# Kernel optimization log

Measured on AMD Instinct MI355X. Metric: run time of the kernel, lower is better.

## Reference

```python
import jax, jax.numpy as jnp
import numpy as np

SEQ_LEN, BATCH, HID, ATT = 2048, 64, 512, 512


def setup_inputs() -> dict:
    key = jax.random.key(0)
    k1, k2, k3, k4, k5, k6 = jax.random.split(key, 6)
    return {
        "dec_out": jax.random.normal(k1, (BATCH, HID), dtype=jnp.float32),
        "enc_outs": jax.random.normal(k2, (SEQ_LEN, BATCH, HID), dtype=jnp.float32),
        "W_s": jax.random.normal(k3, (ATT, HID), dtype=jnp.float32) * (1.0 / np.sqrt(HID)),
        "W_t": jax.random.normal(k4, (ATT, HID), dtype=jnp.float32) * (1.0 / np.sqrt(HID)),
        "b_t": jax.random.normal(k5, (ATT,), dtype=jnp.float32) * 0.01,
        "v_a": jax.random.uniform(k6, (ATT,), dtype=jnp.float32, minval=-0.05, maxval=0.05),
    }


def reference(dec_out, enc_outs, W_s, W_t, b_t, v_a):
    # enc_att: (seq_len, batch, att) = W_s @ enc_outs
    enc_att = jnp.einsum('sbh,ah->sba', enc_outs, W_s)
    # dec_att: (batch, att) = W_t @ dec_out + b_t
    dec_att = dec_out @ W_t.T + b_t
    # score(b, s) = v_a . tanh(enc_att[s,b] + dec_att[b])
    scores = jnp.einsum('sba,a->bs', jnp.tanh(enc_att + dec_att[None, :, :]), v_a)
    return scores  # (batch, seq_len)
```

## Files before the change

kernel.cpp:

```cpp
#include <hip/hip_runtime.h>

typedef __attribute__((ext_vector_type(8))) short short8;
typedef __attribute__((ext_vector_type(4))) float f32x4;

#define SEQ 2048
#define BATCH 64
#define HID 512
#define ATT 512

__device__ __forceinline__ unsigned short f2bf(float f) {
  unsigned u = __float_as_uint(f);
  u += 0x7fffu + ((u >> 16) & 1u);
  return (unsigned short)(u >> 16);
}

__global__ void bahdanau_pre(const float* __restrict__ dec_out,
                             const float* __restrict__ W_t,
                             const float* __restrict__ b_t,
                             const float* __restrict__ W_s,
                             unsigned short* __restrict__ wsb,
                             float* __restrict__ dec_att) {
  if (blockIdx.x < 64) {
    const int b = blockIdx.x;
    __shared__ float drow[HID];
    for (int i = threadIdx.x; i < HID; i += 256) drow[i] = dec_out[b * HID + i];
    __syncthreads();
    for (int a = threadIdx.x; a < ATT; a += 256) {
      const float4* wr = (const float4*)(W_t + (size_t)a * HID);
      float s0 = 0.f, s1 = 0.f, s2 = 0.f, s3 = 0.f;
#pragma unroll 4
      for (int j = 0; j < HID / 4; ++j) {
        float4 w = wr[j];
        s0 = fmaf(w.x, drow[4 * j + 0], s0);
        s1 = fmaf(w.y, drow[4 * j + 1], s1);
        s2 = fmaf(w.z, drow[4 * j + 2], s2);
        s3 = fmaf(w.w, drow[4 * j + 3], s3);
      }
      dec_att[b * ATT + a] = (s0 + s1) + (s2 + s3) + b_t[a];
    }
  } else {
    const int cb = blockIdx.x - 64;
    const float4* src = (const float4*)W_s;
#pragma unroll
    for (int i = 0; i < 4; ++i) {
      int idx = cb * 1024 + i * 256 + threadIdx.x;
      float4 v = src[idx];
      ushort4 o;
      o.x = f2bf(v.x); o.y = f2bf(v.y); o.z = f2bf(v.z); o.w = f2bf(v.w);
      ((ushort4*)wsb)[idx] = o;
    }
  }
}

__global__ __launch_bounds__(512, 2)
void bahdanau_main(const float* __restrict__ enc,
                   const unsigned short* __restrict__ wsb,
                   const float* __restrict__ dec_att,
                   const float* __restrict__ v_a,
                   float* __restrict__ out) {
  __shared__ __align__(16) unsigned short Alds[2][2048];
  __shared__ float partial[8 * 64];

  const int tid  = threadIdx.x;
  const int wave = tid >> 6;
  const int lane = tid & 63;
  const int c = lane & 15;
  const int q = lane >> 4;
  const int s = blockIdx.x;
  const int n0 = wave * 64;

  const int srow = tid >> 3;
  const int skc  = (tid & 7) * 4;
  const int ldst = ((skc >> 3) * 64 + srow) * 8 + (skc & 7);
  const float* gsrc = enc + ((size_t)s * 64 + srow) * HID + skc;

  const unsigned short* bsrc = wsb + (size_t)(n0 + c) * HID + q * 8;

  f32x4 acc[4][4] = {};

  {
    float4 v = *(const float4*)gsrc;
    ushort4 o;
    o.x = f2bf(v.x); o.y = f2bf(v.y); o.z = f2bf(v.z); o.w = f2bf(v.w);
    *(ushort4*)&Alds[0][ldst] = o;
  }
  short8 bp[4];
#pragma unroll
  for (int nt = 0; nt < 4; ++nt)
    bp[nt] = *(const short8*)(bsrc + (size_t)nt * 16 * HID);
  __syncthreads();

#pragma unroll
  for (int kk = 0; kk < 16; ++kk) {
    const int cur = kk & 1;

    short8 bfr[4];
#pragma unroll
    for (int nt = 0; nt < 4; ++nt) bfr[nt] = bp[nt];

    float4 stg;
    if (kk < 15) stg = *(const float4*)(gsrc + (kk + 1) * 32);

    if (kk < 15) {
#pragma unroll
      for (int nt = 0; nt < 4; ++nt)
        bp[nt] = *(const short8*)(bsrc + (size_t)nt * 16 * HID + (kk + 1) * 32);
    }

    const unsigned short* ab = &Alds[cur][(q * 64 + c) * 8];
    short8 a[4];
#pragma unroll
    for (int mt = 0; mt < 4; ++mt)
      a[mt] = *(const short8*)(ab + mt * 16 * 8);

#pragma unroll
    for (int mt = 0; mt < 4; ++mt)
#pragma unroll
      for (int nt = 0; nt < 4; ++nt)
        acc[mt][nt] = __builtin_amdgcn_mfma_f32_16x16x32_bf16(a[mt], bfr[nt], acc[mt][nt], 0, 0, 0);

    if (kk < 15) {
      ushort4 o;
      o.x = f2bf(stg.x); o.y = f2bf(stg.y); o.z = f2bf(stg.z); o.w = f2bf(stg.w);
      *(ushort4*)&Alds[cur ^ 1][ldst] = o;
    }
    __syncthreads();
  }

  float va[4];
#pragma unroll
  for (int nt = 0; nt < 4; ++nt) va[nt] = v_a[n0 + nt * 16 + c];

  float rowsum[4][4];
#pragma unroll
  for (int mt = 0; mt < 4; ++mt) {
#pragma unroll
    for (int r = 0; r < 4; ++r) {
      const int ml = mt * 16 + q * 4 + r;
      float sum = 0.f;
#pragma unroll
      for (int nt = 0; nt < 4; ++nt) {
        const int n = n0 + nt * 16 + c;
        float x = acc[mt][nt][r] + dec_att[ml * ATT + n];
        float e = __builtin_amdgcn_exp2f(x * 2.8853900817779268f);
        float t = 1.f - 2.f * __builtin_amdgcn_rcpf(e + 1.f);
        sum = fmaf(va[nt], t, sum);
      }
      rowsum[mt][r] = sum;
    }
  }

#pragma unroll
  for (int off = 1; off < 16; off <<= 1) {
#pragma unroll
    for (int mt = 0; mt < 4; ++mt)
#pragma unroll
      for (int r = 0; r < 4; ++r)
        rowsum[mt][r] += __shfl_xor(rowsum[mt][r], off, 64);
  }

  if (c == 0) {
#pragma unroll
    for (int mt = 0; mt < 4; ++mt)
#pragma unroll
      for (int r = 0; r < 4; ++r)
        partial[wave * 64 + mt * 16 + q * 4 + r] = rowsum[mt][r];
  }
  __syncthreads();

  if (tid < 64) {
    float sum = 0.f;
#pragma unroll
    for (int w = 0; w < 8; ++w) sum += partial[w * 64 + tid];
    out[(size_t)tid * SEQ + s] = sum;
  }
}

extern "C" void kernel_launch(void* const* d_in, const int* in_sizes, int n_in,
                              void* d_out, int out_size, void* d_ws, size_t ws_size,
                              hipStream_t stream) {
  const float* dec_out = (const float*)d_in[0];
  const float* enc     = (const float*)d_in[1];
  const float* W_s     = (const float*)d_in[2];
  const float* W_t     = (const float*)d_in[3];
  const float* b_t     = (const float*)d_in[4];
  const float* v_a     = (const float*)d_in[5];
  float* out = (float*)d_out;

  unsigned short* wsb = (unsigned short*)d_ws;
  float* dec_att = (float*)((char*)d_ws + (size_t)ATT * HID * 2);

  bahdanau_pre<<<128, 256, 0, stream>>>(dec_out, W_t, b_t, W_s, wsb, dec_att);
  bahdanau_main<<<SEQ, 512, 0, stream>>>(enc, wsb, dec_att, v_a, out);
}
```

Baseline: 532.9 us.

## Process several sequence steps per block with whole-tile register prefetch

Each block now handles 8 sequence positions instead of one. The full 64x512 encoder slab is prefetched into registers, converted to bf16 into a single padded LDS buffer, and the next slab is loaded while the current MFMA loop runs. dec_att is cached once per block in LDS as bf16, and W_s fragments use a two-deep register prefetch. This removes per-k-step barriers and amortizes dec_att reads, at the cost of heavy register pressure (64 floats of staging), large LDS use that lowers occupancy, only 256 blocks, and bf16 rounding of dec_att.

```diff
diff --git a/kernel.cpp b/kernel.cpp
--- a/kernel.cpp
+++ b/kernel.cpp
@@ -7,11 +7,16 @@
 #define BATCH 64
 #define HID 512
 #define ATT 512
+#define SPB 8
+#define DPF 2
 
 __device__ __forceinline__ unsigned short f2bf(float f) {
   unsigned u = __float_as_uint(f);
   u += 0x7fffu + ((u >> 16) & 1u);
   return (unsigned short)(u >> 16);
+}
+__device__ __forceinline__ float bf2f(unsigned short h) {
+  return __uint_as_float(((unsigned)h) << 16);
 }
 
 __global__ void bahdanau_pre(const float* __restrict__ dec_out,
@@ -58,121 +63,144 @@
                    const float* __restrict__ dec_att,
                    const float* __restrict__ v_a,
                    float* __restrict__ out) {
-  __shared__ __align__(16) unsigned short Alds[2][2048];
-  __shared__ float partial[8 * 64];
+  __shared__ __align__(16) unsigned short Albuf[64 * 65 * 8];
+  __shared__ __align__(16) unsigned short decl[64 * 520];
+  __shared__ float partial[512];
 
   const int tid  = threadIdx.x;
   const int wave = tid >> 6;
   const int lane = tid & 63;
   const int c = lane & 15;
   const int q = lane >> 4;
-  const int s = blockIdx.x;
   const int n0 = wave * 64;
+  const int s0 = blockIdx.x * SPB;
+
+  {
+    const float4* dsrc = (const float4*)dec_att;
+#pragma unroll
+    for (int i = 0; i < 16; ++i) {
+      int idx = i * 512 + tid;
+      float4 v = dsrc[idx];
+      int e = idx * 4;
+      int row = e >> 9, col = e & 511;
+      ushort4 o;
+      o.x = f2bf(v.x); o.y = f2bf(v.y); o.z = f2bf(v.z); o.w = f2bf(v.w);
+      *(ushort4*)&decl[row * 520 + col] = o;
+    }
+  }
 
   const int srow = tid >> 3;
   const int skc  = (tid & 7) * 4;
-  const int ldst = ((skc >> 3) * 64 + srow) * 8 + (skc & 7);
-  const float* gsrc = enc + ((size_t)s * 64 + srow) * HID + skc;
+  const int ldst = (((skc >> 3) & 3) * 65 + srow) * 8 + (skc & 7);
+  const float* gbase = enc + ((size_t)s0 * 64 + srow) * HID + skc;
+
+  float4 stg[16];
+#pragma unroll
+  for (int kk = 0; kk < 16; ++kk) stg[kk] = *(const float4*)(gbase + kk * 32);
 
   const unsigned short* bsrc = wsb + (size_t)(n0 + c) * HID + q * 8;
 
-  f32x4 acc[4][4] = {};
-
-  {
-    float4 v = *(const float4*)gsrc;
-    ushort4 o;
-    o.x = f2bf(v.x); o.y = f2bf(v.y); o.z = f2bf(v.z); o.w = f2bf(v.w);
-    *(ushort4*)&Alds[0][ldst] = o;
-  }
-  short8 bp[4];
-#pragma unroll
-  for (int nt = 0; nt < 4; ++nt)
-    bp[nt] = *(const short8*)(bsrc + (size_t)nt * 16 * HID);
+  float va[4];
+#pragma unroll
+  for (int nt = 0; nt < 4; ++nt) va[nt] = v_a[n0 + nt * 16 + c];
+
+  for (int si = 0; si < SPB; ++si) {
+    __syncthreads();
+
+    if (si > 0 && tid < 64) {
+      float sum = 0.f;
+#pragma unroll
+      for (int w = 0; w < 8; ++w) sum += partial[w * 64 + tid];
+      out[(size_t)tid * SEQ + (s0 + si - 1)] = sum;
+    }
+
+#pragma unroll
+    for (int kk = 0; kk < 16; ++kk) {
+      ushort4 o;
+      o.x = f2bf(stg[kk].x); o.y = f2bf(stg[kk].y);
+      o.z = f2bf(stg[kk].z); o.w = f2bf(stg[kk].w);
+      *(ushort4*)&Albuf[kk * 2080 + ldst] = o;
+    }
+
+    __syncthreads();
+
+    const float* gnext = gbase + (size_t)(si + 1) * (64 * HID);
+    const bool more = (si + 1 < SPB);
+
+    short8 bp[DPF][4];
+#pragma unroll
+    for (int d = 0; d < DPF; ++d)
+#pragma unroll
+      for (int nt = 0; nt < 4; ++nt)
+        bp[d][nt] = *(const short8*)(bsrc + (size_t)nt * 16 * HID + d * 32);
+
+    f32x4 acc[4][4] = {};
+
+#pragma unroll
+    for (int kk = 0; kk < 16; ++kk) {
+      const unsigned short* ab = &Albuf[kk * 2080 + (q * 65 + c) * 8];
+      short8 a4[4];
+#pragma unroll
+      for (int mt = 0; mt < 4; ++mt)
+        a4[mt] = *(const short8*)(ab + mt * 16 * 8);
+
+#pragma unroll
+      for (int mt = 0; mt < 4; ++mt)
+#pragma unroll
+        for (int nt = 0; nt < 4; ++nt)
+          acc[mt][nt] = __builtin_amdgcn_mfma_f32_16x16x32_bf16(a4[mt], bp[kk % DPF][nt], acc[mt][nt], 0, 0, 0);
+
+      if (kk + DPF < 16) {
+#pragma unroll
+        for (int nt = 0; nt < 4; ++nt)
+          bp[kk % DPF][nt] = *(const short8*)(bsrc + (size_t)nt * 16 * HID + (kk + DPF) * 32);
+      }
+      if (more) stg[kk] = *(const float4*)(gnext + kk * 32);
+    }
+
+    float rowsum[4][4];
+#pragma unroll
+    for (int mt = 0; mt < 4; ++mt) {
+#pragma unroll
+      for (int r = 0; r < 4; ++r) {
+        const int ml = mt * 16 + q * 4 + r;
+        float sum = 0.f;
+#pragma unroll
+        for (int nt = 0; nt < 4; ++nt) {
+          const int n = n0 + nt * 16 + c;
+          float x = acc[mt][nt][r] + bf2f(decl[ml * 520 + n]);
+          float e = __builtin_amdgcn_exp2f(x * 2.8853900817779268f);
+          float t = 1.f - 2.f * __builtin_amdgcn_rcpf(e + 1.f);
+          sum = fmaf(va[nt], t, sum);
+        }
+        rowsum[mt][r] = sum;
+      }
+    }
+
+#pragma unroll
+    for (int off = 1; off < 16; off <<= 1) {
+#pragma unroll
+      for (int mt = 0; mt < 4; ++mt)
+#pragma unroll
+        for (int r = 0; r < 4; ++r)
+          rowsum[mt][r] += __shfl_xor(rowsum[mt][r], off, 64);
+    }
+
+    if (c == 0) {
+#pragma unroll
+      for (int mt = 0; mt < 4; ++mt)
+#pragma unroll
+        for (int r = 0; r < 4; ++r)
+          partial[wave * 64 + mt * 16 + q * 4 + r] = rowsum[mt][r];
+    }
+  }
+
   __syncthreads();
-
-#pragma unroll
-  for (int kk = 0; kk < 16; ++kk) {
-    const int cur = kk & 1;
-
-    short8 bfr[4];
-#pragma unroll
-    for (int nt = 0; nt < 4; ++nt) bfr[nt] = bp[nt];
-
-    float4 stg;
-    if (kk < 15) stg = *(const float4*)(gsrc + (kk + 1) * 32);
-
-    if (kk < 15) {
-#pragma unroll
-      for (int nt = 0; nt < 4; ++nt)
-        bp[nt] = *(const short8*)(bsrc + (size_t)nt * 16 * HID + (kk + 1) * 32);
-    }
-
-    const unsigned short* ab = &Alds[cur][(q * 64 + c) * 8];
-    short8 a[4];
-#pragma unroll
-    for (int mt = 0; mt < 4; ++mt)
-      a[mt] = *(const short8*)(ab + mt * 16 * 8);
-
-#pragma unroll
-    for (int mt = 0; mt < 4; ++mt)
-#pragma unroll
-      for (int nt = 0; nt < 4; ++nt)
-        acc[mt][nt] = __builtin_amdgcn_mfma_f32_16x16x32_bf16(a[mt], bfr[nt], acc[mt][nt], 0, 0, 0);
-
-    if (kk < 15) {
-      ushort4 o;
-      o.x = f2bf(stg.x); o.y = f2bf(stg.y); o.z = f2bf(stg.z); o.w = f2bf(stg.w);
-      *(ushort4*)&Alds[cur ^ 1][ldst] = o;
-    }
-    __syncthreads();
-  }
-
-  float va[4];
-#pragma unroll
-  for (int nt = 0; nt < 4; ++nt) va[nt] = v_a[n0 + nt * 16 + c];
-
-  float rowsum[4][4];
-#pragma unroll
-  for (int mt = 0; mt < 4; ++mt) {
-#pragma unroll
-    for (int r = 0; r < 4; ++r) {
-      const int ml = mt * 16 + q * 4 + r;
-      float sum = 0.f;
-#pragma unroll
-      for (int nt = 0; nt < 4; ++nt) {
-        const int n = n0 + nt * 16 + c;
-        float x = acc[mt][nt][r] + dec_att[ml * ATT + n];
-        float e = __builtin_amdgcn_exp2f(x * 2.8853900817779268f);
-        float t = 1.f - 2.f * __builtin_amdgcn_rcpf(e + 1.f);
-        sum = fmaf(va[nt], t, sum);
-      }
-      rowsum[mt][r] = sum;
-    }
-  }
-
-#pragma unroll
-  for (int off = 1; off < 16; off <<= 1) {
-#pragma unroll
-    for (int mt = 0; mt < 4; ++mt)
-#pragma unroll
-      for (int r = 0; r < 4; ++r)
-        rowsum[mt][r] += __shfl_xor(rowsum[mt][r], off, 64);
-  }
-
-  if (c == 0) {
-#pragma unroll
-    for (int mt = 0; mt < 4; ++mt)
-#pragma unroll
-      for (int r = 0; r < 4; ++r)
-        partial[wave * 64 + mt * 16 + q * 4 + r] = rowsum[mt][r];
-  }
-  __syncthreads();
-
   if (tid < 64) {
     float sum = 0.f;
 #pragma unroll
     for (int w = 0; w < 8; ++w) sum += partial[w * 64 + tid];
-    out[(size_t)tid * SEQ + s] = sum;
+    out[(size_t)tid * SEQ + (s0 + SPB - 1)] = sum;
   }
 }
 
@@ -191,5 +219,5 @@
   float* dec_att = (float*)((char*)d_ws + (size_t)ATT * HID * 2);
 
   bahdanau_pre<<<128, 256, 0, stream>>>(dec_out, W_t, b_t, W_s, wsb, dec_att);
-  bahdanau_main<<<SEQ, 512, 0, stream>>>(enc, wsb, dec_att, v_a, out);
-}
+  bahdanau_main<<<SEQ / SPB, 512, 0, stream>>>(enc, wsb, dec_att, v_a, out);
+}
```

Result: no change. 542.5 us (+1.8%).

## Stage A and B tiles via global_load_lds DMA and prelayout W_s in MFMA order

Applied to the files above, without the earlier changes.

Replaces the register-staged loads of the fp32 encoder tile and the bf16 W_s fragments with direct global-to-LDS DMA (global_load_lds), double-buffered across the K loop. W_s is pre-permuted in the prep kernel into an MFMA-fragment-friendly blocked layout so each wave copies contiguous 1KB chunks. dec_att is stored transposed and used to initialize the accumulators, removing the scattered adds in the epilogue. The main kernel now needs 80KB of LDS, which may cut occupancy below the launch-bounds target of two blocks per CU, and the bf16 conversion of A now happens after the LDS read.

```diff
diff --git a/kernel.cpp b/kernel.cpp
--- a/kernel.cpp
+++ b/kernel.cpp
@@ -12,6 +12,12 @@
   unsigned u = __float_as_uint(f);
   u += 0x7fffu + ((u >> 16) & 1u);
   return (unsigned short)(u >> 16);
+}
+
+__device__ __forceinline__ void dma16(const void* g, void* l) {
+  __builtin_amdgcn_global_load_lds(
+      (const __attribute__((address_space(1))) unsigned int*)g,
+      (__attribute__((address_space(3))) unsigned int*)l, 16, 0, 0);
 }
 
 __global__ void bahdanau_pre(const float* __restrict__ dec_out,
@@ -19,7 +25,7 @@
                              const float* __restrict__ b_t,
                              const float* __restrict__ W_s,
                              unsigned short* __restrict__ wsb,
-                             float* __restrict__ dec_att) {
+                             float* __restrict__ decT) {
   if (blockIdx.x < 64) {
     const int b = blockIdx.x;
     __shared__ float drow[HID];
@@ -36,7 +42,7 @@
         s2 = fmaf(w.z, drow[4 * j + 2], s2);
         s3 = fmaf(w.w, drow[4 * j + 3], s3);
       }
-      dec_att[b * ATT + a] = (s0 + s1) + (s2 + s3) + b_t[a];
+      decT[a * BATCH + b] = (s0 + s1) + (s2 + s3) + b_t[a];
     }
   } else {
     const int cb = blockIdx.x - 64;
@@ -45,9 +51,13 @@
     for (int i = 0; i < 4; ++i) {
       int idx = cb * 1024 + i * 256 + threadIdx.x;
       float4 v = src[idx];
+      int a = idx >> 7;
+      int h = (idx & 127) * 4;
       ushort4 o;
       o.x = f2bf(v.x); o.y = f2bf(v.y); o.z = f2bf(v.z); o.w = f2bf(v.w);
-      ((ushort4*)wsb)[idx] = o;
+      int blk = (a >> 4) * 64 + ((h >> 3) & 3) * 16 + (a & 15);
+      int dst = (h >> 5) * 16384 + blk * 8 + (h & 7);
+      *(ushort4*)&wsb[dst] = o;
     }
   }
 }
@@ -55,93 +65,95 @@
 __global__ __launch_bounds__(512, 2)
 void bahdanau_main(const float* __restrict__ enc,
                    const unsigned short* __restrict__ wsb,
-                   const float* __restrict__ dec_att,
+                   const float* __restrict__ decT,
                    const float* __restrict__ v_a,
                    float* __restrict__ out) {
-  __shared__ __align__(16) unsigned short Alds[2][2048];
-  __shared__ float partial[8 * 64];
+  __shared__ __align__(16) unsigned char smem[81920];
+  unsigned short* Bb[2] = { (unsigned short*)smem, (unsigned short*)(smem + 32768) };
+  float* Ab[2] = { (float*)(smem + 65536), (float*)(smem + 73728) };
+  float* partial = (float*)(smem + 65536);
 
   const int tid  = threadIdx.x;
-  const int wave = tid >> 6;
+  const int w    = tid >> 6;
   const int lane = tid & 63;
   const int c = lane & 15;
   const int q = lane >> 4;
   const int s = blockIdx.x;
-  const int n0 = wave * 64;
-
-  const int srow = tid >> 3;
-  const int skc  = (tid & 7) * 4;
-  const int ldst = ((skc >> 3) * 64 + srow) * 8 + (skc & 7);
-  const float* gsrc = enc + ((size_t)s * 64 + srow) * HID + skc;
-
-  const unsigned short* bsrc = wsb + (size_t)(n0 + c) * HID + q * 8;
-
-  f32x4 acc[4][4] = {};
-
-  {
-    float4 v = *(const float4*)gsrc;
-    ushort4 o;
-    o.x = f2bf(v.x); o.y = f2bf(v.y); o.z = f2bf(v.z); o.w = f2bf(v.w);
-    *(ushort4*)&Alds[0][ldst] = o;
-  }
-  short8 bp[4];
+  const int n0 = w * 64;
+
+  const char* encB = (const char*)(enc + (size_t)s * 64 * HID);
+  const char* wsbB = (const char*)wsb;
+
+  const int am = (w & 3) * 16 + (lane & 15);
+  const int ag = (lane >> 4) * 2 + (w >> 2);
+  const char* aSrc = encB + am * 2048 + ag * 16;
+
+  f32x4 acc[4][4];
 #pragma unroll
   for (int nt = 0; nt < 4; ++nt)
-    bp[nt] = *(const short8*)(bsrc + (size_t)nt * 16 * HID);
-  __syncthreads();
-
-#pragma unroll
-  for (int kk = 0; kk < 16; ++kk) {
-    const int cur = kk & 1;
-
-    short8 bfr[4];
-#pragma unroll
-    for (int nt = 0; nt < 4; ++nt) bfr[nt] = bp[nt];
-
-    float4 stg;
-    if (kk < 15) stg = *(const float4*)(gsrc + (kk + 1) * 32);
-
-    if (kk < 15) {
+#pragma unroll
+    for (int mt = 0; mt < 4; ++mt)
+      acc[mt][nt] = *(const f32x4*)(decT + (size_t)(n0 + nt * 16 + c) * 64 + mt * 16 + q * 4);
+
+  float va[4];
+#pragma unroll
+  for (int nt = 0; nt < 4; ++nt) va[nt] = v_a[n0 + nt * 16 + c];
+
+  dma16(aSrc, (char*)Ab[0] + w * 1024);
+#pragma unroll
+  for (int d = 0; d < 4; ++d)
+    dma16(wsbB + w * 4096 + d * 1024 + lane * 16, (char*)Bb[0] + w * 4096 + d * 1024);
+
+#pragma unroll
+  for (int kb = 0; kb < 16; ++kb) {
+    const int cur = kb & 1;
+    __syncthreads();
+
+    if (kb < 15) {
+      const int nb = kb + 1;
+      const int nxt = nb & 1;
+      dma16(aSrc + nb * 128, (char*)Ab[nxt] + w * 1024);
+#pragma unroll
+      for (int d = 0; d < 4; ++d)
+        dma16(wsbB + nb * 32768 + w * 4096 + d * 1024 + lane * 16,
+              (char*)Bb[nxt] + w * 4096 + d * 1024);
+    }
+
+    const float* Ac = Ab[cur];
+    const unsigned short* Bc = Bb[cur];
+    short8 af[4];
+#pragma unroll
+    for (int mt = 0; mt < 4; ++mt) {
+      float4 lo = *(const float4*)(Ac + (mt * 64 + q * 16 + c) * 4);
+      float4 hi = *(const float4*)(Ac + (256 + mt * 64 + q * 16 + c) * 4);
+      short8 t;
+      t[0] = (short)f2bf(lo.x); t[1] = (short)f2bf(lo.y);
+      t[2] = (short)f2bf(lo.z); t[3] = (short)f2bf(lo.w);
+      t[4] = (short)f2bf(hi.x); t[5] = (short)f2bf(hi.y);
+      t[6] = (short)f2bf(hi.z); t[7] = (short)f2bf(hi.w);
+      af[mt] = t;
+    }
+    short8 bf[4];
+#pragma unroll
+    for (int nt = 0; nt < 4; ++nt)
+      bf[nt] = *(const short8*)(Bc + (((w * 4 + nt) * 64 + q * 16 + c) * 8));
+
+#pragma unroll
+    for (int mt = 0; mt < 4; ++mt)
 #pragma unroll
       for (int nt = 0; nt < 4; ++nt)
-        bp[nt] = *(const short8*)(bsrc + (size_t)nt * 16 * HID + (kk + 1) * 32);
-    }
-
-    const unsigned short* ab = &Alds[cur][(q * 64 + c) * 8];
-    short8 a[4];
-#pragma unroll
-    for (int mt = 0; mt < 4; ++mt)
-      a[mt] = *(const short8*)(ab + mt * 16 * 8);
-
-#pragma unroll
-    for (int mt = 0; mt < 4; ++mt)
-#pragma unroll
-      for (int nt = 0; nt < 4; ++nt)
-        acc[mt][nt] = __builtin_amdgcn_mfma_f32_16x16x32_bf16(a[mt], bfr[nt], acc[mt][nt], 0, 0, 0);
-
-    if (kk < 15) {
-      ushort4 o;
-      o.x = f2bf(stg.x); o.y = f2bf(stg.y); o.z = f2bf(stg.z); o.w = f2bf(stg.w);
-      *(ushort4*)&Alds[cur ^ 1][ldst] = o;
-    }
-    __syncthreads();
-  }
-
-  float va[4];
-#pragma unroll
-  for (int nt = 0; nt < 4; ++nt) va[nt] = v_a[n0 + nt * 16 + c];
+        acc[mt][nt] = __builtin_amdgcn_mfma_f32_16x16x32_bf16(af[mt], bf[nt], acc[mt][nt], 0, 0, 0);
+  }
 
   float rowsum[4][4];
 #pragma unroll
   for (int mt = 0; mt < 4; ++mt) {
 #pragma unroll
     for (int r = 0; r < 4; ++r) {
-      const int ml = mt * 16 + q * 4 + r;
       float sum = 0.f;
 #pragma unroll
       for (int nt = 0; nt < 4; ++nt) {
-        const int n = n0 + nt * 16 + c;
-        float x = acc[mt][nt][r] + dec_att[ml * ATT + n];
+        float x = acc[mt][nt][r];
         float e = __builtin_amdgcn_exp2f(x * 2.8853900817779268f);
         float t = 1.f - 2.f * __builtin_amdgcn_rcpf(e + 1.f);
         sum = fmaf(va[nt], t, sum);
@@ -164,14 +176,14 @@
     for (int mt = 0; mt < 4; ++mt)
 #pragma unroll
       for (int r = 0; r < 4; ++r)
-        partial[wave * 64 + mt * 16 + q * 4 + r] = rowsum[mt][r];
+        partial[w * 64 + mt * 16 + q * 4 + r] = rowsum[mt][r];
   }
   __syncthreads();
 
   if (tid < 64) {
     float sum = 0.f;
 #pragma unroll
-    for (int w = 0; w < 8; ++w) sum += partial[w * 64 + tid];
+    for (int ww = 0; ww < 8; ++ww) sum += partial[ww * 64 + tid];
     out[(size_t)tid * SEQ + s] = sum;
   }
 }
@@ -188,8 +200,8 @@
   float* out = (float*)d_out;
 
   unsigned short* wsb = (unsigned short*)d_ws;
-  float* dec_att = (float*)((char*)d_ws + (size_t)ATT * HID * 2);
-
-  bahdanau_pre<<<128, 256, 0, stream>>>(dec_out, W_t, b_t, W_s, wsb, dec_att);
-  bahdanau_main<<<SEQ, 512, 0, stream>>>(enc, wsb, dec_att, v_a, out);
-}
+  float* decT = (float*)((char*)d_ws + (size_t)ATT * HID * 2);
+
+  bahdanau_pre<<<128, 256, 0, stream>>>(dec_out, W_t, b_t, W_s, wsb, decT);
+  bahdanau_main<<<SEQ, 512, 0, stream>>>(enc, wsb, decT, v_a, out);
+}
```

New measurement: 491.2 us. 7.8% less time.
